# Kernel optimization log

Hardware: AMD Instinct MI355X
Metric: run time of the kernel (lower is better)

## Reference

```python
import jax, jax.numpy as jnp
import numpy as np

D_MODEL = 768
HEAD_SIZE = 64

def setup_inputs() -> dict:
    key = jax.random.key(0)
    ks = jax.random.split(key, 7)
    B, S = 8, 2048
    x = jax.random.normal(ks[0], (B, S, D_MODEL), dtype=jnp.float32)
    s = 1.0 / np.sqrt(D_MODEL)
    Wq = jax.random.uniform(ks[1], (D_MODEL, HEAD_SIZE), jnp.float32, -s, s)
    bq = jnp.zeros((HEAD_SIZE,), jnp.float32)
    Wk = jax.random.uniform(ks[2], (D_MODEL, HEAD_SIZE), jnp.float32, -s, s)
    bk = jnp.zeros((HEAD_SIZE,), jnp.float32)
    Wv = jax.random.uniform(ks[3], (D_MODEL, HEAD_SIZE), jnp.float32, -s, s)
    bv = jnp.zeros((HEAD_SIZE,), jnp.float32)
    return {"x": x, "Wq": Wq, "bq": bq, "Wk": Wk, "bk": bk, "Wv": Wv, "bv": bv}

def reference(x, Wq, bq, Wk, bk, Wv, bv):
    # Single attention head: softmax(Q K^T / sqrt(head_size)) V
    q = jnp.einsum('bsd,dh->bsh', x, Wq) + bq  # [B,S,H]
    k = jnp.einsum('bsd,dh->bsh', x, Wk) + bk
    v = jnp.einsum('bsd,dh->bsh', x, Wv) + bv
    scale = 1.0 / jnp.sqrt(jnp.array(HEAD_SIZE, dtype=x.dtype))
    scores = jnp.einsum('bqh,bkh->bqk', q, k) * scale  # [B,S,S]
    attn = jax.nn.softmax(scores, axis=-1)
    out = jnp.einsum('bqk,bkh->bqh', attn, v)  # [B,S,H]
    return out
```

## Files before the change

kernel.cpp:

```cpp
#include <hip/hip_runtime.h>
#include <math.h>

#define D_MODEL 768
#define HS 64
#define BATCH 8
#define SEQ 2048
#define QSCALE_LOG2E 0.1803368801f
#define KSPLIT 8
#define KCHUNK (SEQ / KSPLIT)
#define PM 32

typedef _Float16 half_t;
typedef __attribute__((ext_vector_type(8))) _Float16 half8;
typedef __attribute__((ext_vector_type(4))) float floatx4;

typedef const __attribute__((address_space(1))) void gas_void;
typedef __attribute__((address_space(3))) void las_void;
__device__ __forceinline__ void gl_lds16(const void* g, void* l) {
    __builtin_amdgcn_global_load_lds((gas_void*)g, (las_void*)l, 16, 0, 0);
}
__device__ __forceinline__ void waitcnt_all() {
    __builtin_amdgcn_s_waitcnt(0);
}
__device__ __forceinline__ float fast_exp2(float x) {
#if __has_builtin(__builtin_amdgcn_exp2f)
    return __builtin_amdgcn_exp2f(x);
#else
    return exp2f(x);
#endif
}

__global__ __launch_bounds__(256)
void wconv_kernel(const float* __restrict__ Wq, const float* __restrict__ Wk,
                  const float* __restrict__ Wv, half_t* __restrict__ Wt)
{
    __shared__ float lds[64][65];
    const int m = blockIdx.x / 12;
    const int k0 = (blockIdx.x % 12) * 64;
    const float* W = (m == 0) ? Wq : ((m == 1) ? Wk : Wv);
    const int tid = threadIdx.x;
#pragma unroll
    for (int ri = 0; ri < 4; ++ri) {
        int row = ri * 16 + (tid >> 4);
        int col = (tid & 15) * 4;
        float4 v = *(const float4*)(W + (size_t)(k0 + row) * HS + col);
        lds[row][col] = v.x; lds[row][col + 1] = v.y;
        lds[row][col + 2] = v.z; lds[row][col + 3] = v.w;
    }
    __syncthreads();
#pragma unroll
    for (int i = 0; i < 2; ++i) {
        int idx = i * 256 + tid;
        int h = idx >> 3;
        int kc = idx & 7;
        half8 o;
#pragma unroll
        for (int j = 0; j < 8; ++j) o[j] = (half_t)lds[kc * 8 + j][h];
        *(half8*)(Wt + (size_t)(m * HS + h) * D_MODEL + k0 + kc * 8) = o;
    }
}

__global__ __launch_bounds__(256)
void proj_kernel(const float* __restrict__ x, const half_t* __restrict__ Wt,
                 const float* __restrict__ bq, const float* __restrict__ bk,
                 const float* __restrict__ bv,
                 half_t* __restrict__ Qh, half_t* __restrict__ Kh,
                 half_t* __restrict__ Vt)
{
    __shared__ __align__(16) half_t xs[2][PM * 64];
    __shared__ __align__(16) half_t wtl[2][192 * 64];

    const int tid = threadIdx.x;
    const int w = tid >> 6;
    const int lane = tid & 63;
    const int l15 = lane & 15;
    const int quad = lane >> 4;
    const long row0 = (long)blockIdx.x * PM;

    floatx4 acc[2][3];
#pragma unroll
    for (int i = 0; i < 2; ++i)
#pragma unroll
        for (int j = 0; j < 3; ++j) acc[i][j] = (floatx4){0.f, 0.f, 0.f, 0.f};

    float4 xA[2], xB[2];

    auto loadx = [&](int k0, float4 (&v)[2]) {
        int r = tid >> 3, sc = tid & 7;
        int cg = sc ^ (r & 7);
        const float* p = x + (row0 + r) * D_MODEL + k0 + cg * 8;
        v[0] = *(const float4*)p;
        v[1] = *(const float4*)(p + 4);
    };
    auto stage_w = [&](int p, int k0) {
#pragma unroll
        for (int i = 0; i < 6; ++i) {
            int idx = i * 256 + tid;
            int r = idx >> 3, sc = idx & 7;
            int cg = sc ^ (r & 7);
            gl_lds16(Wt + (size_t)r * D_MODEL + k0 + cg * 8, &wtl[p][idx * 8]);
        }
    };

    auto step = [&](int it, float4 (&xc)[2], float4 (&xn)[2], int p) {
        {
            float4 a = xc[0], b = xc[1];
            half8 xh = (half8){(half_t)a.x, (half_t)a.y, (half_t)a.z, (half_t)a.w,
                               (half_t)b.x, (half_t)b.y, (half_t)b.z, (half_t)b.w};
            *(half8*)&xs[p][tid * 8] = xh;
        }
        waitcnt_all();
        __syncthreads();
        int kn = (it + 1 < 12) ? (it + 1) * 64 : 0;
        if (it + 1 < 12) stage_w(p ^ 1, kn);
        loadx(kn, xn);
#pragma unroll
        for (int kst = 0; kst < 2; ++kst) {
            half8 af[2];
#pragma unroll
            for (int mt = 0; mt < 2; ++mt) {
                int r = mt * 16 + l15;
                int slot = (kst * 4 + quad) ^ (r & 7);
                af[mt] = *(const half8*)&xs[p][r * 64 + slot * 8];
            }
#pragma unroll
            for (int nt = 0; nt < 3; ++nt) {
                int r = w * 48 + nt * 16 + l15;
                int slot = (kst * 4 + quad) ^ (r & 7);
                half8 bf = *(const half8*)&wtl[p][r * 64 + slot * 8];
#pragma unroll
                for (int mt = 0; mt < 2; ++mt)
                    acc[mt][nt] = __builtin_amdgcn_mfma_f32_16x16x32_f16(
                        af[mt], bf, acc[mt][nt], 0, 0, 0);
            }
        }
    };

    stage_w(0, 0);
    loadx(0, xA);
#pragma unroll
    for (int it = 0; it < 12; it += 2) {
        step(it,     xA, xB, 0);
        step(it + 1, xB, xA, 1);
    }

#pragma unroll
    for (int nt = 0; nt < 3; ++nt) {
        int nbase = w * 48 + nt * 16;
        int mm = nbase >> 6;
        int h = (nbase + l15) & 63;
        const float* bias = (mm == 0) ? bq : ((mm == 1) ? bk : bv);
        float bval = bias[h];
#pragma unroll
        for (int mt = 0; mt < 2; ++mt)
#pragma unroll
            for (int r = 0; r < 4; ++r) {
                long R = row0 + mt * 16 + quad * 4 + r;
                float fv = acc[mt][nt][r] + bval;
                if (mm == 0) {
                    Qh[R * HS + h] = (half_t)(fv * QSCALE_LOG2E);
                } else if (mm == 1) {
                    Kh[R * HS + h] = (half_t)fv;
                } else {
                    long bb = R >> 11, s = R & 2047;
                    Vt[(bb * HS + h) * SEQ + s] = (half_t)fv;
                }
            }
    }
}

__global__ __launch_bounds__(512)
void attn8_kernel(const half_t* __restrict__ Qh, const half_t* __restrict__ Kh,
                  const half_t* __restrict__ Vt, float* __restrict__ out)
{
    __shared__ __align__(16) half_t osl[8][4096 + 32];
    __shared__ float lsl[8][64];

    const int tid = threadIdx.x;
    const int w = tid >> 6;
    const int lane = tid & 63;
    const int l15 = lane & 15;
    const int quad = lane >> 4;
    const int b  = blockIdx.x >> 5;
    const int qt = blockIdx.x & 31;
    const int q0 = qt * 64;
    const int kk_begin = w * KCHUNK;

    const half_t* Kb = Kh + (size_t)b * SEQ * HS;
    const half_t* Vb = Vt + (size_t)b * HS * SEQ;

    half8 qf[4][2];
#pragma unroll
    for (int mt = 0; mt < 4; ++mt)
#pragma unroll
        for (int hst = 0; hst < 2; ++hst)
            qf[mt][hst] = *(const half8*)(Qh + ((size_t)b * SEQ + q0 + mt * 16 + l15) * HS
                                          + hst * 32 + quad * 8);

    floatx4 oacc[4][4];
    float lsum[4];
#pragma unroll
    for (int mt = 0; mt < 4; ++mt) {
#pragma unroll
        for (int nt = 0; nt < 4; ++nt) oacc[mt][nt] = (floatx4){0.f, 0.f, 0.f, 0.f};
        lsum[mt] = 0.f;
    }

    for (int it = 0; it < KCHUNK / 64; ++it) {
        const int kk0 = kk_begin + it * 64;

        half8 vf[4][2];
#pragma unroll
        for (int nt = 0; nt < 4; ++nt)
#pragma unroll
            for (int kst = 0; kst < 2; ++kst)
                vf[nt][kst] = *(const half8*)(Vb + (size_t)(nt * 16 + l15) * SEQ
                                              + kk0 + kst * 32 + quad * 8);

        half8 kfr[4][2];
#pragma unroll
        for (int t = 0; t < 4; ++t) {
            int r = ((t >> 1) << 5) | ((l15 >> 2) << 3) | ((t & 1) << 2) | (l15 & 3);
#pragma unroll
            for (int hst = 0; hst < 2; ++hst)
                kfr[t][hst] = *(const half8*)(Kb + (size_t)(kk0 + r) * HS
                                              + hst * 32 + quad * 8);
        }

#pragma unroll
        for (int h2 = 0; h2 < 2; ++h2) {
            floatx4 sacc[2][4];
#pragma unroll
            for (int mtl = 0; mtl < 2; ++mtl)
#pragma unroll
                for (int t = 0; t < 4; ++t) sacc[mtl][t] = (floatx4){0.f, 0.f, 0.f, 0.f};
#pragma unroll
            for (int t = 0; t < 4; ++t)
#pragma unroll
                for (int hst = 0; hst < 2; ++hst)
#pragma unroll
                    for (int mtl = 0; mtl < 2; ++mtl)
                        sacc[mtl][t] = __builtin_amdgcn_mfma_f32_16x16x32_f16(
                            kfr[t][hst], qf[h2 * 2 + mtl][hst], sacc[mtl][t], 0, 0, 0);

#pragma unroll
            for (int mtl = 0; mtl < 2; ++mtl) {
                int mt = h2 * 2 + mtl;
                union { int i[4]; half8 h; } pa[2];
#pragma unroll
                for (int t = 0; t < 4; ++t)
#pragma unroll
                    for (int pr = 0; pr < 2; ++pr) {
                        float p0 = fast_exp2(sacc[mtl][t][pr * 2]);
                        float p1 = fast_exp2(sacc[mtl][t][pr * 2 + 1]);
                        lsum[mt] += p0 + p1;
                        union { _Float16 hh[2]; int ii; } u;
                        u.hh[0] = (half_t)p0;
                        u.hh[1] = (half_t)p1;
                        pa[t >> 1].i[(t & 1) * 2 + pr] = u.ii;
                    }
#pragma unroll
                for (int kst = 0; kst < 2; ++kst)
#pragma unroll
                    for (int nt = 0; nt < 4; ++nt)
                        oacc[mt][nt] = __builtin_amdgcn_mfma_f32_16x16x32_f16(
                            pa[kst].h, vf[nt][kst], oacc[mt][nt], 0, 0, 0);
            }
        }
    }

#pragma unroll
    for (int mt = 0; mt < 4; ++mt) {
        float s = lsum[mt];
        s += __shfl_xor(s, 16);
        s += __shfl_xor(s, 32);
        lsum[mt] = s;
    }

#pragma unroll
    for (int mt = 0; mt < 4; ++mt)
#pragma unroll
        for (int nt = 0; nt < 4; ++nt)
#pragma unroll
            for (int r = 0; r < 4; ++r) {
                int row = mt * 16 + quad * 4 + r;
                osl[w][row * 64 + nt * 16 + l15] = (half_t)oacc[mt][nt][r];
            }
    if (quad == 0)
#pragma unroll
        for (int mt = 0; mt < 4; ++mt)
            lsl[w][mt * 16 + l15] = lsum[mt];
    __syncthreads();

#pragma unroll
    for (int i = 0; i < 8; ++i) {
        int row = i * 8 + w;
        float s = 0.f, l = 0.f;
#pragma unroll
        for (int s8 = 0; s8 < 8; ++s8) {
            s += (float)osl[s8][row * 64 + lane];
            l += lsl[s8][row];
        }
        out[((size_t)b * SEQ + q0 + row) * HS + lane] = s / l;
    }
}

extern "C" void kernel_launch(void* const* d_in, const int* in_sizes, int n_in,
                              void* d_out, int out_size, void* d_ws, size_t ws_size,
                              hipStream_t stream) {
    const float* x  = (const float*)d_in[0];
    const float* Wq = (const float*)d_in[1];
    const float* bq = (const float*)d_in[2];
    const float* Wk = (const float*)d_in[3];
    const float* bk = (const float*)d_in[4];
    const float* Wv = (const float*)d_in[5];
    const float* bv = (const float*)d_in[6];
    float* out = (float*)d_out;

    const size_t per = (size_t)BATCH * SEQ * HS;
    half_t* Qh = (half_t*)d_ws;
    half_t* Kh = Qh + per;
    half_t* Vt = Kh + per;
    half_t* Wt = Vt + per;

    wconv_kernel<<<dim3(36), dim3(256), 0, stream>>>(Wq, Wk, Wv, Wt);
    proj_kernel<<<dim3(BATCH * SEQ / PM), dim3(256), 0, stream>>>(
        x, Wt, bq, bk, bv, Qh, Kh, Vt);
    attn8_kernel<<<dim3(BATCH * (SEQ / 64)), dim3(512), 0, stream>>>(
        Qh, Kh, Vt, out);
}
```

Before: 125.8 us.

## Load projection operands directly from global memory, dropping LDS double-buffering

The projection kernel no longer stages x and the transposed weights through double-buffered shared memory with async global-to-LDS loads and barriers. Each wave now reads its MFMA fragments straight from global memory, converting x to fp16 in registers. This removes the LDS traffic and the block-wide syncs per k-step. In exchange, x rows get re-read by all four waves, the accesses are less coalesced, and there is no software prefetch to overlap loads with MFMA work.

Result: slower. 148.1 us (+17.7%).

```diff
diff --git a/kernel.cpp b/kernel.cpp
--- a/kernel.cpp
+++ b/kernel.cpp
@@ -14,14 +14,6 @@
 typedef __attribute__((ext_vector_type(8))) _Float16 half8;
 typedef __attribute__((ext_vector_type(4))) float floatx4;
 
-typedef const __attribute__((address_space(1))) void gas_void;
-typedef __attribute__((address_space(3))) void las_void;
-__device__ __forceinline__ void gl_lds16(const void* g, void* l) {
-    __builtin_amdgcn_global_load_lds((gas_void*)g, (las_void*)l, 16, 0, 0);
-}
-__device__ __forceinline__ void waitcnt_all() {
-    __builtin_amdgcn_s_waitcnt(0);
-}
 __device__ __forceinline__ float fast_exp2(float x) {
 #if __has_builtin(__builtin_amdgcn_exp2f)
     return __builtin_amdgcn_exp2f(x);
@@ -67,9 +59,6 @@
                  half_t* __restrict__ Qh, half_t* __restrict__ Kh,
                  half_t* __restrict__ Vt)
 {
-    __shared__ __align__(16) half_t xs[2][PM * 64];
-    __shared__ __align__(16) half_t wtl[2][192 * 64];
-
     const int tid = threadIdx.x;
     const int w = tid >> 6;
     const int lane = tid & 63;
@@ -83,65 +72,35 @@
 #pragma unroll
         for (int j = 0; j < 3; ++j) acc[i][j] = (floatx4){0.f, 0.f, 0.f, 0.f};
 
-    float4 xA[2], xB[2];
-
-    auto loadx = [&](int k0, float4 (&v)[2]) {
-        int r = tid >> 3, sc = tid & 7;
-        int cg = sc ^ (r & 7);
-        const float* p = x + (row0 + r) * D_MODEL + k0 + cg * 8;
-        v[0] = *(const float4*)p;
-        v[1] = *(const float4*)(p + 4);
-    };
-    auto stage_w = [&](int p, int k0) {
-#pragma unroll
-        for (int i = 0; i < 6; ++i) {
-            int idx = i * 256 + tid;
-            int r = idx >> 3, sc = idx & 7;
-            int cg = sc ^ (r & 7);
-            gl_lds16(Wt + (size_t)r * D_MODEL + k0 + cg * 8, &wtl[p][idx * 8]);
-        }
-    };
-
-    auto step = [&](int it, float4 (&xc)[2], float4 (&xn)[2], int p) {
-        {
-            float4 a = xc[0], b = xc[1];
-            half8 xh = (half8){(half_t)a.x, (half_t)a.y, (half_t)a.z, (half_t)a.w,
-                               (half_t)b.x, (half_t)b.y, (half_t)b.z, (half_t)b.w};
-            *(half8*)&xs[p][tid * 8] = xh;
-        }
-        waitcnt_all();
-        __syncthreads();
-        int kn = (it + 1 < 12) ? (it + 1) * 64 : 0;
-        if (it + 1 < 12) stage_w(p ^ 1, kn);
-        loadx(kn, xn);
-#pragma unroll
-        for (int kst = 0; kst < 2; ++kst) {
-            half8 af[2];
-#pragma unroll
-            for (int mt = 0; mt < 2; ++mt) {
-                int r = mt * 16 + l15;
-                int slot = (kst * 4 + quad) ^ (r & 7);
-                af[mt] = *(const half8*)&xs[p][r * 64 + slot * 8];
-            }
-#pragma unroll
-            for (int nt = 0; nt < 3; ++nt) {
-                int r = w * 48 + nt * 16 + l15;
-                int slot = (kst * 4 + quad) ^ (r & 7);
-                half8 bf = *(const half8*)&wtl[p][r * 64 + slot * 8];
+    for (int it = 0; it < 12; ++it) {
+        const int k0 = it * 64;
+        half8 af[2][2];
+#pragma unroll
+        for (int mt = 0; mt < 2; ++mt)
+#pragma unroll
+            for (int kst = 0; kst < 2; ++kst) {
+                const float* p = x + (row0 + mt * 16 + l15) * D_MODEL
+                                 + k0 + kst * 32 + quad * 8;
+                float4 a = *(const float4*)p;
+                float4 c = *(const float4*)(p + 4);
+                af[mt][kst] = (half8){(half_t)a.x, (half_t)a.y, (half_t)a.z, (half_t)a.w,
+                                      (half_t)c.x, (half_t)c.y, (half_t)c.z, (half_t)c.w};
+            }
+        half8 bf[3][2];
+#pragma unroll
+        for (int nt = 0; nt < 3; ++nt)
+#pragma unroll
+            for (int kst = 0; kst < 2; ++kst)
+                bf[nt][kst] = *(const half8*)(Wt + (size_t)(w * 48 + nt * 16 + l15) * D_MODEL
+                                              + k0 + kst * 32 + quad * 8);
+#pragma unroll
+        for (int kst = 0; kst < 2; ++kst)
+#pragma unroll
+            for (int nt = 0; nt < 3; ++nt)
 #pragma unroll
                 for (int mt = 0; mt < 2; ++mt)
                     acc[mt][nt] = __builtin_amdgcn_mfma_f32_16x16x32_f16(
-                        af[mt], bf, acc[mt][nt], 0, 0, 0);
-            }
-        }
-    };
-
-    stage_w(0, 0);
-    loadx(0, xA);
-#pragma unroll
-    for (int it = 0; it < 12; it += 2) {
-        step(it,     xA, xB, 0);
-        step(it + 1, xB, xA, 1);
+                        af[mt][kst], bf[nt][kst], acc[mt][nt], 0, 0, 0);
     }
 
 #pragma unroll
```
